# Optimization experiments

Measured on AMD Instinct MI355X. Metric: run time of the kernel, lower is better.

Reference implementation:

```python
import jax, jax.numpy as jnp
import numpy as np

B, S, H = 16, 4096, 1024

def setup_inputs() -> dict:
    key = jax.random.key(0)
    k1, k2, k3 = jax.random.split(key, 3)
    lstm_output = jax.random.normal(k1, (B, S, H), dtype=jnp.float32)
    # nn.Linear(H, H): weight [H, H] (out, in), bias [H]
    W = jax.random.normal(k2, (H, H), dtype=jnp.float32) * (1.0 / np.sqrt(H))
    b = jax.random.normal(k3, (H,), dtype=jnp.float32) * 0.01
    return {"lstm_output": lstm_output, "W": W, "b": b}

def reference(lstm_output, W, b):
    # energy = tanh(x @ W^T + b)  [B, S, H]
    energy = jnp.tanh(jnp.einsum('bsh,oh->bso', lstm_output, W) + b)
    # softmax over the sequence dim (dim=1), per hidden channel
    scores = jax.nn.softmax(energy, axis=1)
    # weighted-sum pooling over sequence -> [B, H]
    context = jnp.sum(scores * lstm_output, axis=1)
    return context
```

## Files before the change

### kernel.cpp

```cpp
#include <hip/hip_runtime.h>
#include <hip/hip_bf16.h>

#define Bsz  16
#define Sdim 4096
#define Hdim 1024
#define Mtot (Bsz * Sdim)
#define Kdim Hdim
#define Ndim Hdim
#define BM 128
#define BN 128
#define BK 32
#define MT (Mtot / BM)
#define NT (Ndim / BN)
#define NKT (Kdim / BK)

typedef short s16x8 __attribute__((ext_vector_type(8)));
typedef float f32x4 __attribute__((ext_vector_type(4)));

__device__ __forceinline__ unsigned short f2bf(float f) {
  __hip_bfloat16 h = __float2bfloat16(f);
  unsigned short u;
  __builtin_memcpy(&u, &h, 2);
  return u;
}

__device__ __forceinline__ s16x8 cvt8(float4 u, float4 v) {
  s16x8 r;
  r[0] = (short)f2bf(u.x); r[1] = (short)f2bf(u.y);
  r[2] = (short)f2bf(u.z); r[3] = (short)f2bf(u.w);
  r[4] = (short)f2bf(v.x); r[5] = (short)f2bf(v.y);
  r[6] = (short)f2bf(v.z); r[7] = (short)f2bf(v.w);
  return r;
}

__global__ __launch_bounds__(256) void wconv_kernel(const float* __restrict__ W,
                                                    unsigned short* __restrict__ Wb) {
  int i = blockIdx.x * 256 + threadIdx.x;
  float4 v = reinterpret_cast<const float4*>(W)[i];
  ushort4 o;
  o.x = f2bf(v.x); o.y = f2bf(v.y); o.z = f2bf(v.z); o.w = f2bf(v.w);
  reinterpret_cast<ushort4*>(Wb)[i] = o;
}

__global__ __launch_bounds__(256) void attn_main(
    const float* __restrict__ X,
    const unsigned short* __restrict__ Wb,
    const float* __restrict__ bias,
    float* __restrict__ lpart,
    float* __restrict__ cpart) {
  __shared__ unsigned short Al[BM * BK];
  __shared__ unsigned short Bl[BN * BK];
  __shared__ float red[2][2][BN];

  int bid = blockIdx.x;
  int swz = (bid & 7) * (MT * NT / 8) + (bid >> 3);
  int mt = swz >> 3;
  int nt = swz & 7;
  const int m0 = mt * BM;
  const int n0 = nt * BN;

  const int tid  = threadIdx.x;
  const int lane = tid & 63;
  const int wave = tid >> 6;
  const int wm = wave >> 1, wn = wave & 1;
  const int lr = lane & 15, lk = lane >> 4;

  f32x4 acc[4][4];
#pragma unroll
  for (int i = 0; i < 4; i++)
#pragma unroll
    for (int j = 0; j < 4; j++) acc[i][j] = (f32x4){0.f, 0.f, 0.f, 0.f};

  const int srow_st = tid >> 1;
  const int scol_st = (tid & 1) * 16;
  const float*          Ag = X  + (size_t)(m0 + srow_st) * Kdim + scol_st;
  const unsigned short* Bg = Wb + (size_t)(n0 + srow_st) * Kdim + scol_st;

  float4 a0 = *(const float4*)(Ag + 0);
  float4 a1 = *(const float4*)(Ag + 4);
  float4 a2 = *(const float4*)(Ag + 8);
  float4 a3 = *(const float4*)(Ag + 12);
  s16x8  b0 = *(const s16x8*)(Bg + 0);
  s16x8  b1 = *(const s16x8*)(Bg + 8);

  for (int kt = 0; kt < NKT; ++kt) {
    __syncthreads();
    *(s16x8*)&Al[srow_st * BK + scol_st]     = cvt8(a0, a1);
    *(s16x8*)&Al[srow_st * BK + scol_st + 8] = cvt8(a2, a3);
    *(s16x8*)&Bl[srow_st * BK + scol_st]     = b0;
    *(s16x8*)&Bl[srow_st * BK + scol_st + 8] = b1;
    __syncthreads();

    if (kt + 1 < NKT) {
      const float* ap = Ag + (kt + 1) * BK;
      a0 = *(const float4*)(ap);
      a1 = *(const float4*)(ap + 4);
      a2 = *(const float4*)(ap + 8);
      a3 = *(const float4*)(ap + 12);
      const unsigned short* bp = Bg + (kt + 1) * BK;
      b0 = *(const s16x8*)(bp);
      b1 = *(const s16x8*)(bp + 8);
    }

    s16x8 af[4], bfr[4];
#pragma unroll
    for (int mr = 0; mr < 4; mr++)
      af[mr] = *(const s16x8*)&Al[(wm * 64 + mr * 16 + lr) * BK + lk * 8];
#pragma unroll
    for (int nr = 0; nr < 4; nr++)
      bfr[nr] = *(const s16x8*)&Bl[(wn * 64 + nr * 16 + lr) * BK + lk * 8];
#pragma unroll
    for (int mr = 0; mr < 4; mr++)
#pragma unroll
      for (int nr = 0; nr < 4; nr++)
        acc[mr][nr] = __builtin_amdgcn_mfma_f32_16x16x32_bf16(af[mr], bfr[nr], acc[mr][nr], 0, 0, 0);
  }

  float lsum[4], csum[4];
#pragma unroll
  for (int nr = 0; nr < 4; nr++) {
    const int o = n0 + wn * 64 + nr * 16 + lr;
    const float bv = bias[o];
    float lacc = 0.f, cacc = 0.f;
#pragma unroll
    for (int mr = 0; mr < 4; mr++) {
      const int srow = m0 + wm * 64 + mr * 16 + lk * 4;
#pragma unroll
      for (int r = 0; r < 4; r++) {
        float e  = acc[mr][nr][r] + bv;
        float t  = __expf(2.f * e);
        float th = 1.f - __fdividef(2.f, t + 1.f);
        float sc = __expf(th);
        float xv = X[(size_t)(srow + r) * Kdim + o];
        lacc += sc;
        cacc += sc * xv;
      }
    }
    lacc += __shfl_xor(lacc, 16); lacc += __shfl_xor(lacc, 32);
    cacc += __shfl_xor(cacc, 16); cacc += __shfl_xor(cacc, 32);
    lsum[nr] = lacc; csum[nr] = cacc;
  }

  if (lk == 0) {
#pragma unroll
    for (int nr = 0; nr < 4; nr++) {
      red[wm][0][wn * 64 + nr * 16 + lr] = lsum[nr];
      red[wm][1][wn * 64 + nr * 16 + lr] = csum[nr];
    }
  }
  __syncthreads();
  if (tid < BN) {
    float L = red[0][0][tid] + red[1][0][tid];
    float C = red[0][1][tid] + red[1][1][tid];
    lpart[(size_t)mt * Ndim + n0 + tid] = L;
    cpart[(size_t)mt * Ndim + n0 + tid] = C;
  }
}

__global__ __launch_bounds__(256) void finalize_kernel(const float* __restrict__ lpart,
                                                       const float* __restrict__ cpart,
                                                       float* __restrict__ out) {
  int i = blockIdx.x * 256 + threadIdx.x;
  int b = i >> 10, o = i & 1023;
  float L = 0.f, C = 0.f;
#pragma unroll 4
  for (int sc = 0; sc < Sdim / BM; ++sc) {
    size_t idx = (size_t)(b * (Sdim / BM) + sc) * Ndim + o;
    L += lpart[idx];
    C += cpart[idx];
  }
  out[i] = C / L;
}

extern "C" void kernel_launch(void* const* d_in, const int* in_sizes, int n_in,
                              void* d_out, int out_size, void* d_ws, size_t ws_size,
                              hipStream_t stream) {
  const float* X    = (const float*)d_in[0];
  const float* W    = (const float*)d_in[1];
  const float* bias = (const float*)d_in[2];
  float* out = (float*)d_out;

  unsigned short* Wb = (unsigned short*)d_ws;
  float* lpart = (float*)((char*)d_ws + (size_t)Ndim * Kdim * 2);
  float* cpart = lpart + (size_t)MT * Ndim;

  wconv_kernel<<<dim3(Ndim * Kdim / 1024), dim3(256), 0, stream>>>(W, Wb);
  attn_main<<<dim3(MT * NT), dim3(256), 0, stream>>>(X, Wb, bias, lpart, cpart);
  finalize_kernel<<<dim3(Bsz * Hdim / 256), dim3(256), 0, stream>>>(lpart, cpart, out);
}
```

Measured before the change: 296.2 us.

## Pre-convert activations to bf16 and stream GEMM tiles directly into LDS

Adds a pass that converts the whole fp32 input X to bf16 in workspace. The main kernel then loads bf16 tiles straight into LDS with global_load_lds, replacing the register-staged fp32 loads and in-kernel conversion. The epilogue also reads bf16 X for the weighted sum, which halves the activation bytes but lowers the precision of the context accumulation. The old path is kept as a fallback when the workspace is too small. The extra conversion pass reads and writes the full activation tensor, and the new loop loses the prior register prefetch overlap.

Result: slower. 308.2 us (+4.0%).

```diff
diff --git a/kernel.cpp b/kernel.cpp
--- a/kernel.cpp
+++ b/kernel.cpp
@@ -23,6 +23,11 @@
   __builtin_memcpy(&u, &h, 2);
   return u;
 }
+__device__ __forceinline__ float bf2f(unsigned short u) {
+  __hip_bfloat16 h;
+  __builtin_memcpy(&h, &u, 2);
+  return __bfloat162float(h);
+}
 
 __device__ __forceinline__ s16x8 cvt8(float4 u, float4 v) {
   s16x8 r;
@@ -33,6 +38,21 @@
   return r;
 }
 
+__device__ __forceinline__ void gload_lds16(const unsigned short* g, unsigned short* l) {
+  __builtin_amdgcn_global_load_lds(
+      (const __attribute__((address_space(1))) unsigned int*)g,
+      (__attribute__((address_space(3))) unsigned int*)l,
+      16, 0, 0);
+}
+
+__global__ __launch_bounds__(256) void xconv_kernel(const float* __restrict__ X,
+                                                    unsigned short* __restrict__ Xb) {
+  size_t i = (size_t)blockIdx.x * 256 + threadIdx.x;
+  float4 u = reinterpret_cast<const float4*>(X)[2 * i];
+  float4 v = reinterpret_cast<const float4*>(X)[2 * i + 1];
+  reinterpret_cast<s16x8*>(Xb)[i] = cvt8(u, v);
+}
+
 __global__ __launch_bounds__(256) void wconv_kernel(const float* __restrict__ W,
                                                     unsigned short* __restrict__ Wb) {
   int i = blockIdx.x * 256 + threadIdx.x;
@@ -43,7 +63,7 @@
 }
 
 __global__ __launch_bounds__(256) void attn_main(
-    const float* __restrict__ X,
+    const unsigned short* __restrict__ Xb,
     const unsigned short* __restrict__ Wb,
     const float* __restrict__ bias,
     float* __restrict__ lpart,
@@ -71,18 +91,103 @@
 #pragma unroll
     for (int j = 0; j < 4; j++) acc[i][j] = (f32x4){0.f, 0.f, 0.f, 0.f};
 
-  const int srow_st = tid >> 1;
-  const int scol_st = (tid & 1) * 16;
+  const int srow = wave * 32 + (lane >> 2);
+  const int scol = (lane & 3) * 8;
+  const unsigned short* Ag0 = Xb + (size_t)(m0 + srow) * Kdim + scol;
+  const unsigned short* Ag1 = Ag0 + (size_t)16 * Kdim;
+  const unsigned short* Bg0 = Wb + (size_t)(n0 + srow) * Kdim + scol;
+  const unsigned short* Bg1 = Bg0 + (size_t)16 * Kdim;
+  unsigned short* Alw = &Al[wave * 1024];
+  unsigned short* Blw = &Bl[wave * 1024];
+
+  for (int kt = 0; kt < NKT; ++kt) {
+    const int ko = kt * BK;
+    gload_lds16(Ag0 + ko, Alw);
+    gload_lds16(Ag1 + ko, Alw + 512);
+    gload_lds16(Bg0 + ko, Blw);
+    gload_lds16(Bg1 + ko, Blw + 512);
+    __syncthreads();
+
+    s16x8 af[4], bfr[4];
+#pragma unroll
+    for (int mr = 0; mr < 4; mr++)
+      af[mr] = *(const s16x8*)&Al[(wm * 64 + mr * 16 + lr) * BK + lk * 8];
+#pragma unroll
+    for (int nr = 0; nr < 4; nr++)
+      bfr[nr] = *(const s16x8*)&Bl[(wn * 64 + nr * 16 + lr) * BK + lk * 8];
+#pragma unroll
+    for (int mr = 0; mr < 4; mr++)
+#pragma unroll
+      for (int nr = 0; nr < 4; nr++)
+        acc[mr][nr] = __builtin_amdgcn_mfma_f32_16x16x32_bf16(af[mr], bfr[nr], acc[mr][nr], 0, 0, 0);
+
+    __syncthreads();
+  }
+
+  float lsum[4], csum[4];
+#pragma unroll
+  for (int nr = 0; nr < 4; nr++) {
+    const int o = n0 + wn * 64 + nr * 16 + lr;
+    const float bv = bias[o];
+    float lacc = 0.f, cacc = 0.f;
+#pragma unroll
+    for (int mr = 0; mr < 4; mr++) {
+      const int sr = m0 + wm * 64 + mr * 16 + lk * 4;
+#pragma unroll
+      for (int r = 0; r < 4; r++) {
+        float e  = acc[mr][nr][r] + bv;
+        float t  = __expf(2.f * e);
+        float th = 1.f - __fdividef(2.f, t + 1.f);
+        float sc = __expf(th);
+        float xv = bf2f(Xb[(size_t)(sr + r) * Kdim + o]);
+        lacc += sc;
+        cacc += sc * xv;
+      }
+    }
+    lacc += __shfl_xor(lacc, 16); lacc += __shfl_xor(lacc, 32);
+    cacc += __shfl_xor(cacc, 16); cacc += __shfl_xor(cacc, 32);
+    lsum[nr] = lacc; csum[nr] = cacc;
+  }
+
+  if (lk == 0) {
+#pragma unroll
+    for (int nr = 0; nr < 4; nr++) {
+      red[wm][0][wn * 64 + nr * 16 + lr] = lsum[nr];
+      red[wm][1][wn * 64 + nr * 16 + lr] = csum[nr];
+    }
+  }
+  __syncthreads();
+  if (tid < BN) {
+    float L = red[0][0][tid] + red[1][0][tid];
+    float C = red[0][1][tid] + red[1][1][tid];
+    lpart[(size_t)mt * Ndim + n0 + tid] = L;
+    cpart[(size_t)mt * Ndim + n0 + tid] = C;
+  }
+}
+
+__global__ __launch_bounds__(256) void attn_main_fb(
+    const float* __restrict__ X, const unsigned short* __restrict__ Wb,
+    const float* __restrict__ bias, float* __restrict__ lpart, float* __restrict__ cpart) {
+  __shared__ unsigned short Al[BM * BK];
+  __shared__ unsigned short Bl[BN * BK];
+  __shared__ float red[2][2][BN];
+  int bid = blockIdx.x;
+  int swz = (bid & 7) * (MT * NT / 8) + (bid >> 3);
+  int mt = swz >> 3, nt = swz & 7;
+  const int m0 = mt * BM, n0 = nt * BN;
+  const int tid = threadIdx.x, lane = tid & 63, wave = tid >> 6;
+  const int wm = wave >> 1, wn = wave & 1, lr = lane & 15, lk = lane >> 4;
+  f32x4 acc[4][4];
+#pragma unroll
+  for (int i = 0; i < 4; i++)
+#pragma unroll
+    for (int j = 0; j < 4; j++) acc[i][j] = (f32x4){0.f, 0.f, 0.f, 0.f};
+  const int srow_st = tid >> 1, scol_st = (tid & 1) * 16;
   const float*          Ag = X  + (size_t)(m0 + srow_st) * Kdim + scol_st;
   const unsigned short* Bg = Wb + (size_t)(n0 + srow_st) * Kdim + scol_st;
-
-  float4 a0 = *(const float4*)(Ag + 0);
-  float4 a1 = *(const float4*)(Ag + 4);
-  float4 a2 = *(const float4*)(Ag + 8);
-  float4 a3 = *(const float4*)(Ag + 12);
-  s16x8  b0 = *(const s16x8*)(Bg + 0);
-  s16x8  b1 = *(const s16x8*)(Bg + 8);
-
+  float4 a0 = *(const float4*)(Ag + 0), a1 = *(const float4*)(Ag + 4);
+  float4 a2 = *(const float4*)(Ag + 8), a3 = *(const float4*)(Ag + 12);
+  s16x8 b0 = *(const s16x8*)(Bg + 0), b1 = *(const s16x8*)(Bg + 8);
   for (int kt = 0; kt < NKT; ++kt) {
     __syncthreads();
     *(s16x8*)&Al[srow_st * BK + scol_st]     = cvt8(a0, a1);
@@ -90,18 +195,13 @@
     *(s16x8*)&Bl[srow_st * BK + scol_st]     = b0;
     *(s16x8*)&Bl[srow_st * BK + scol_st + 8] = b1;
     __syncthreads();
-
     if (kt + 1 < NKT) {
       const float* ap = Ag + (kt + 1) * BK;
-      a0 = *(const float4*)(ap);
-      a1 = *(const float4*)(ap + 4);
-      a2 = *(const float4*)(ap + 8);
-      a3 = *(const float4*)(ap + 12);
+      a0 = *(const float4*)(ap);     a1 = *(const float4*)(ap + 4);
+      a2 = *(const float4*)(ap + 8); a3 = *(const float4*)(ap + 12);
       const unsigned short* bp = Bg + (kt + 1) * BK;
-      b0 = *(const s16x8*)(bp);
-      b1 = *(const s16x8*)(bp + 8);
-    }
-
+      b0 = *(const s16x8*)(bp);      b1 = *(const s16x8*)(bp + 8);
+    }
     s16x8 af[4], bfr[4];
 #pragma unroll
     for (int mr = 0; mr < 4; mr++)
@@ -115,7 +215,6 @@
       for (int nr = 0; nr < 4; nr++)
         acc[mr][nr] = __builtin_amdgcn_mfma_f32_16x16x32_bf16(af[mr], bfr[nr], acc[mr][nr], 0, 0, 0);
   }
-
   float lsum[4], csum[4];
 #pragma unroll
   for (int nr = 0; nr < 4; nr++) {
@@ -124,23 +223,21 @@
     float lacc = 0.f, cacc = 0.f;
 #pragma unroll
     for (int mr = 0; mr < 4; mr++) {
-      const int srow = m0 + wm * 64 + mr * 16 + lk * 4;
+      const int sr = m0 + wm * 64 + mr * 16 + lk * 4;
 #pragma unroll
       for (int r = 0; r < 4; r++) {
         float e  = acc[mr][nr][r] + bv;
         float t  = __expf(2.f * e);
         float th = 1.f - __fdividef(2.f, t + 1.f);
         float sc = __expf(th);
-        float xv = X[(size_t)(srow + r) * Kdim + o];
-        lacc += sc;
-        cacc += sc * xv;
+        float xv = X[(size_t)(sr + r) * Kdim + o];
+        lacc += sc; cacc += sc * xv;
       }
     }
     lacc += __shfl_xor(lacc, 16); lacc += __shfl_xor(lacc, 32);
     cacc += __shfl_xor(cacc, 16); cacc += __shfl_xor(cacc, 32);
     lsum[nr] = lacc; csum[nr] = cacc;
   }
-
   if (lk == 0) {
 #pragma unroll
     for (int nr = 0; nr < 4; nr++) {
@@ -180,11 +277,26 @@
   const float* bias = (const float*)d_in[2];
   float* out = (float*)d_out;
 
-  unsigned short* Wb = (unsigned short*)d_ws;
-  float* lpart = (float*)((char*)d_ws + (size_t)Ndim * Kdim * 2);
-  float* cpart = lpart + (size_t)MT * Ndim;
-
-  wconv_kernel<<<dim3(Ndim * Kdim / 1024), dim3(256), 0, stream>>>(W, Wb);
-  attn_main<<<dim3(MT * NT), dim3(256), 0, stream>>>(X, Wb, bias, lpart, cpart);
-  finalize_kernel<<<dim3(Bsz * Hdim / 256), dim3(256), 0, stream>>>(lpart, cpart, out);
-}
+  const size_t xb_bytes = (size_t)Mtot * Kdim * 2;
+  const size_t wb_bytes = (size_t)Ndim * Kdim * 2;
+  const size_t lp_bytes = (size_t)MT * Ndim * 4;
+  const size_t need = xb_bytes + wb_bytes + 2 * lp_bytes;
+
+  if (ws_size >= need) {
+    unsigned short* Xb = (unsigned short*)d_ws;
+    unsigned short* Wb = (unsigned short*)((char*)d_ws + xb_bytes);
+    float* lpart = (float*)((char*)d_ws + xb_bytes + wb_bytes);
+    float* cpart = lpart + (size_t)MT * Ndim;
+    xconv_kernel<<<dim3(Mtot * (Kdim / 8) / 256), dim3(256), 0, stream>>>(X, Xb);
+    wconv_kernel<<<dim3(Ndim * Kdim / 1024), dim3(256), 0, stream>>>(W, Wb);
+    attn_main<<<dim3(MT * NT), dim3(256), 0, stream>>>(Xb, Wb, bias, lpart, cpart);
+    finalize_kernel<<<dim3(Bsz * Hdim / 256), dim3(256), 0, stream>>>(lpart, cpart, out);
+  } else {
+    unsigned short* Wb = (unsigned short*)d_ws;
+    float* lpart = (float*)((char*)d_ws + wb_bytes);
+    float* cpart = lpart + (size_t)MT * Ndim;
+    wconv_kernel<<<dim3(Ndim * Kdim / 1024), dim3(256), 0, stream>>>(W, Wb);
+    attn_main_fb<<<dim3(MT * NT), dim3(256), 0, stream>>>(X, Wb, bias, lpart, cpart);
+    finalize_kernel<<<dim3(Bsz * Hdim / 256), dim3(256), 0, stream>>>(lpart, cpart, out);
+  }
+}
```
